# Optimization experiments

Measured on AMD Instinct MI355X. Metric: run time of the kernel, lower is better.

## Reference

```python
import jax, jax.numpy as jnp
import numpy as np

B, S, N = 8, 2048, 1024

def setup_inputs() -> dict:
    key = jax.random.key(0)
    k1, k2, k3 = jax.random.split(key, 3)
    outer = jax.random.normal(k1, (B, S, N), dtype=jnp.float32)
    extended_attention_mask = jnp.zeros((B, 1, S), dtype=jnp.float32)
    # torch Linear init scale ~ 1/sqrt(n)
    sc = 1.0 / np.sqrt(N)
    Wk = jax.random.normal(k2, (N, N), dtype=jnp.float32) * sc
    bk = jnp.zeros((N,), dtype=jnp.float32)
    Wq = jax.random.normal(k3, (N, N), dtype=jnp.float32) * sc
    bq = jnp.zeros((N,), dtype=jnp.float32)
    return {"outer": outer, "extended_attention_mask": extended_attention_mask,
            "Wk": Wk, "bk": bk, "Wq": Wq, "bq": bq}

def reference(outer, extended_attention_mask, Wk, bk, Wq, bq):
    # k = sigmoid(outer @ Wk^T + bk), q = sigmoid(outer @ Wq^T + bq)
    k = jax.nn.sigmoid(jnp.einsum('bsn,mn->bsm', outer, Wk) + bk)  # [B,S,N]
    q = jax.nn.sigmoid(jnp.einsum('bsn,mn->bsm', outer, Wq) + bq)  # [B,S,N]
    # scores: q @ k^T + mask -> [B,S,S]
    s = jnp.einsum('bqn,bkn->bqk', q, k) + extended_attention_mask
    attn = jax.nn.softmax(s, axis=-1)
    out = jnp.einsum('bqk,bkn->bqn', attn, outer)  # [B,S,N]
    return out.sum(-1)  # [B,S]
```

## Files before the change

### kernel.cpp

```cpp
#include <hip/hip_runtime.h>
#include <hip/hip_bf16.h>

#define BB 8
#define SS 2048
#define NN 1024
#define MT (BB*SS)
#define NPC 32

typedef __attribute__((ext_vector_type(8))) short bf16x8;
typedef __attribute__((ext_vector_type(4))) float f32x4;
typedef unsigned short u16;
typedef unsigned int u32;

__device__ __forceinline__ u16 f2bf(float f) {
  u32 u = __float_as_uint(f);
  u += 0x7fff + ((u >> 16) & 1);
  return (u16)(u >> 16);
}
__device__ __forceinline__ float bf2f(u16 h) {
  return __uint_as_float(((u32)h) << 16);
}

typedef __attribute__((address_space(1))) void GV;
typedef __attribute__((address_space(3))) void LV;
__device__ __forceinline__ void cp16(const void* g, void* l) {
  __builtin_amdgcn_global_load_lds((GV*)g, (LV*)l, 16, 0, 0);
}

__global__ __launch_bounds__(256) void prep_kernel(const float* __restrict__ outer,
                                                   const float* __restrict__ mask,
                                                   const float* __restrict__ Wq,
                                                   const float* __restrict__ Wk,
                                                   const float* __restrict__ bq,
                                                   const float* __restrict__ bk,
                                                   u16* __restrict__ Xb,
                                                   float* __restrict__ r,
                                                   float* __restrict__ kb,
                                                   u16* __restrict__ Wb,
                                                   float* __restrict__ bb) {
  int blk = blockIdx.x;
  if (blk < MT / 4) {
    int w = threadIdx.x >> 6, lane = threadIdx.x & 63;
    int row = blk * 4 + w;
    const float4* src = (const float4*)(outer + (size_t)row * NN);
    ushort4* dst = (ushort4*)(Xb + (size_t)row * NN);
    float s = 0.f;
#pragma unroll
    for (int u = 0; u < 4; u++) {
      int idx = lane + u * 64;
      float4 v = src[idx];
      ushort4 o;
      o.x = f2bf(v.x); o.y = f2bf(v.y); o.z = f2bf(v.z); o.w = f2bf(v.w);
      dst[idx] = o;
      s += (v.x + v.y) + (v.z + v.w);
    }
#pragma unroll
    for (int off = 1; off < 64; off <<= 1) s += __shfl_xor(s, off);
    if (lane == 0) { r[row] = s; kb[row] = mask[row]; }
  } else {
    int idx = (blk - MT / 4) * 256 + threadIdx.x;
    int e = idx * 4;
    int rowm = e >> 10;
    int col = e & 1023;
    const float* srcp = (rowm < NN) ? (Wq + (size_t)rowm * NN + col)
                                    : (Wk + (size_t)(rowm - NN) * NN + col);
    float4 v = *(const float4*)srcp;
    ushort4 o; o.x = f2bf(v.x); o.y = f2bf(v.y); o.z = f2bf(v.z); o.w = f2bf(v.w);
    *(ushort4*)(Wb + (size_t)e) = o;
    if (idx < 2 * NN) bb[idx] = (idx < NN) ? bq[idx] : bk[idx - NN];
  }
}

__global__ __launch_bounds__(256, 4) void gemm1_kernel(const u16* __restrict__ X,
                                                       const u16* __restrict__ W,
                                                       const float* __restrict__ bb,
                                                       u16* __restrict__ C,
                                                       float* __restrict__ kb) {
  __shared__ u16 lA[128 * 32];
  __shared__ u16 lB[128 * 32];
  int bid = blockIdx.x;
  int tn = ((bid & 7) << 1) | ((bid >> 3) & 1);
  int tm = bid >> 4;
  int tid = threadIdx.x;
  int w = tid >> 6, lane = tid & 63;
  int wr = w >> 1, wc = w & 1;
  int srow = tid >> 2;
  int gchunk = (tid & 3) ^ ((tid >> 3) & 3);
  const u16* gA = X + (size_t)(tm * 128 + srow) * NN + gchunk * 8;
  const u16* gB = W + (size_t)(tn * 128 + srow) * NN + gchunk * 8;
  u16* dA = &lA[srow * 32 + (tid & 3) * 8];
  u16* dB = &lB[srow * 32 + (tid & 3) * 8];
  int quad = lane >> 4;
  int rl = lane & 15;
  int sw = quad ^ ((rl >> 1) & 3);
  const u16* pa0 = &lA[(wr * 64 + rl) * 32 + sw * 8];
  const u16* pb0 = &lB[(wc * 64 + rl) * 32 + sw * 8];
  f32x4 acc[4][4] = {};
  for (int kk = 0; kk < NN; kk += 32) {
    cp16(gA, dA);
    cp16(gA + 64 * NN, dA + 64 * 32);
    cp16(gB, dB);
    cp16(gB + 64 * NN, dB + 64 * 32);
    gA += 32; gB += 32;
    __syncthreads();
    bf16x8 af[4], bf[4];
#pragma unroll
    for (int i = 0; i < 4; i++) af[i] = *(const bf16x8*)(pa0 + i * 16 * 32);
#pragma unroll
    for (int j = 0; j < 4; j++) bf[j] = *(const bf16x8*)(pb0 + j * 16 * 32);
#pragma unroll
    for (int i = 0; i < 4; i++)
#pragma unroll
      for (int j = 0; j < 4; j++)
        acc[i][j] = __builtin_amdgcn_mfma_f32_16x16x32_bf16(af[i], bf[j], acc[i][j], 0, 0, 0);
    __syncthreads();
  }
  int quad4 = quad * 4;
  int colb = tn * 128 + wc * 64 + rl;
  bool khalf = (tn >= 8);
#pragma unroll
  for (int i = 0; i < 4; i++) {
    float rsum[4] = {0.f, 0.f, 0.f, 0.f};
#pragma unroll
    for (int j = 0; j < 4; j++) {
      int col = colb + j * 16;
      float bias = bb[col];
#pragma unroll
      for (int rg = 0; rg < 4; rg++) {
        int row = tm * 128 + wr * 64 + i * 16 + quad4 + rg;
        float v = acc[i][j][rg] + bias;
        float sg = 1.0f / (1.0f + __expf(-v));
        u16 h = f2bf(sg - 0.5f);
        C[(size_t)row * 2048 + col] = h;
        rsum[rg] += bf2f(h);
      }
    }
    if (khalf) {
#pragma unroll
      for (int rg = 0; rg < 4; rg++) {
        float s = rsum[rg];
#pragma unroll
        for (int off = 1; off < 16; off <<= 1) s += __shfl_xor(s, off);
        if (rl == 0) {
          int row = tm * 128 + wr * 64 + i * 16 + quad4 + rg;
          atomicAdd(&kb[row], 0.5f * s);
        }
      }
    }
  }
}

__global__ __launch_bounds__(256, 4) void flash_kernel(const u16* __restrict__ C,
                                                       const float* __restrict__ kb,
                                                       const float* __restrict__ r,
                                                       float* __restrict__ pm,
                                                       float* __restrict__ pl,
                                                       float* __restrict__ pt) {
  __shared__ u16 lA[128 * 32];
  __shared__ u16 lB[128 * 32];
  int bid = blockIdx.x;
  int b  = bid & 7;
  int kc = (bid >> 3) & 15;
  int qt = bid >> 7;
  int tid = threadIdx.x;
  int w = tid >> 6, lane = tid & 63;
  int wr = w >> 1, wc = w & 1;
  int srow = tid >> 2;
  int gchunk = (tid & 3) ^ ((tid >> 3) & 3);
  int key0 = kc * 128;
  const u16* gA = C + (size_t)(b * SS + qt * 128 + srow) * 2048 + gchunk * 8;
  const u16* gB = C + (size_t)(b * SS + key0 + srow) * 2048 + 1024 + gchunk * 8;
  u16* dA = &lA[srow * 32 + (tid & 3) * 8];
  u16* dB = &lB[srow * 32 + (tid & 3) * 8];
  int quad = lane >> 4;
  int rl = lane & 15;
  int sw = quad ^ ((rl >> 1) & 3);
  const u16* pa0 = &lA[(wr * 64 + rl) * 32 + sw * 8];
  const u16* pb0 = &lB[(wc * 64 + rl) * 32 + sw * 8];

  f32x4 acc[4][4] = {};
  for (int kk = 0; kk < NN; kk += 32) {
    cp16(gA, dA);
    cp16(gA + 64 * 2048, dA + 64 * 32);
    cp16(gB, dB);
    cp16(gB + 64 * 2048, dB + 64 * 32);
    gA += 32; gB += 32;
    __syncthreads();
    bf16x8 af[4], bf[4];
#pragma unroll
    for (int i = 0; i < 4; i++) af[i] = *(const bf16x8*)(pa0 + i * 16 * 32);
#pragma unroll
    for (int j = 0; j < 4; j++) bf[j] = *(const bf16x8*)(pb0 + j * 16 * 32);
#pragma unroll
    for (int i = 0; i < 4; i++)
#pragma unroll
      for (int j = 0; j < 4; j++)
        acc[i][j] = __builtin_amdgcn_mfma_f32_16x16x32_bf16(af[i], bf[j], acc[i][j], 0, 0, 0);
    __syncthreads();
  }

  float kbv[4], rv[4];
  int colg = b * SS + key0 + wc * 64 + rl;
#pragma unroll
  for (int j = 0; j < 4; j++) { kbv[j] = kb[colg + j * 16]; rv[j] = r[colg + j * 16]; }
  int quad4 = quad * 4;
  int chunk = kc * 2 + wc;
#pragma unroll
  for (int i = 0; i < 4; i++) {
#pragma unroll
    for (int rg = 0; rg < 4; rg++) {
      float lg[4];
      float tmax = -1e30f;
#pragma unroll
      for (int j = 0; j < 4; j++) { lg[j] = acc[i][j][rg] + kbv[j]; tmax = fmaxf(tmax, lg[j]); }
#pragma unroll
      for (int off = 1; off < 16; off <<= 1) tmax = fmaxf(tmax, __shfl_xor(tmax, off));
      float rs = 0.f, rt = 0.f;
#pragma unroll
      for (int j = 0; j < 4; j++) {
        float p = __expf(lg[j] - tmax);
        rs += p; rt += p * rv[j];
      }
#pragma unroll
      for (int off = 1; off < 16; off <<= 1) { rs += __shfl_xor(rs, off); rt += __shfl_xor(rt, off); }
      if (rl == 0) {
        int grow = b * SS + qt * 128 + wr * 64 + i * 16 + quad4 + rg;
        pm[grow * NPC + chunk] = tmax;
        pl[grow * NPC + chunk] = rs;
        pt[grow * NPC + chunk] = rt;
      }
    }
  }
}

__global__ __launch_bounds__(256) void fixup_kernel(const float* __restrict__ pm,
                                                    const float* __restrict__ pl,
                                                    const float* __restrict__ pt,
                                                    float* __restrict__ out) {
  int row = blockIdx.x * 256 + threadIdx.x;
  float Mx = -1e30f;
#pragma unroll
  for (int c = 0; c < NPC; c++) Mx = fmaxf(Mx, pm[row * NPC + c]);
  float L = 0.f, T = 0.f;
#pragma unroll
  for (int c = 0; c < NPC; c++) {
    float a = __expf(pm[row * NPC + c] - Mx);
    L += pl[row * NPC + c] * a;
    T += pt[row * NPC + c] * a;
  }
  out[row] = T / L;
}

extern "C" void kernel_launch(void* const* d_in, const int* in_sizes, int n_in,
                              void* d_out, int out_size, void* d_ws, size_t ws_size,
                              hipStream_t stream) {
  const float* outer = (const float*)d_in[0];
  const float* mask  = (const float*)d_in[1];
  const float* Wk    = (const float*)d_in[2];
  const float* bk    = (const float*)d_in[3];
  const float* Wq    = (const float*)d_in[4];
  const float* bq    = (const float*)d_in[5];
  float* out = (float*)d_out;

  char* ws = (char*)d_ws;
  size_t off = 0;
  auto alloc = [&](size_t bytes) -> void* {
    void* p = ws + off;
    off = (off + bytes + 255) & ~(size_t)255;
    return p;
  };
  u16* Xb  = (u16*)alloc((size_t)MT * NN * 2);
  u16* Wb  = (u16*)alloc((size_t)2048 * NN * 2);
  u16* Cq  = (u16*)alloc((size_t)MT * 2048 * 2);
  float* bb = (float*)alloc(2048 * 4);
  float* rr = (float*)alloc((size_t)MT * 4);
  float* kb = (float*)alloc((size_t)MT * 4);
  float* pm = (float*)alloc((size_t)MT * NPC * 4);
  float* pl = (float*)alloc((size_t)MT * NPC * 4);
  float* pt = (float*)alloc((size_t)MT * NPC * 4);

  prep_kernel<<<dim3(MT / 4 + 2048), dim3(256), 0, stream>>>(outer, mask, Wq, Wk, bq, bk,
                                                             Xb, rr, kb, Wb, bb);
  gemm1_kernel<<<dim3(2048), dim3(256), 0, stream>>>(Xb, Wb, bb, Cq, kb);
  flash_kernel<<<dim3(2048), dim3(256), 0, stream>>>(Cq, kb, rr, pm, pl, pt);
  fixup_kernel<<<dim3(MT / 256), dim3(256), 0, stream>>>(pm, pl, pt, out);
}
```

Before: 295.5 us.

## Fuse fixup into flash kernel via last-block counter and remap gemm tiles

Removes the separate fixup kernel: each flash block bumps an atomic counter per (batch, query-tile), and the last of the 16 arriving blocks merges the partial max/sum/weighted-sum for its 128 rows. This saves one kernel launch and its reload of the partials, at the cost of a memset and fences. The gemm1 block-to-tile mapping is also changed so that blocks sharing an XCD get distinct M tiles and iterate over all N tiles, aiming at better L2 reuse of X. The launch-bounds occupancy hint drops from 4 to 3 blocks for gemm1 and flash, giving the compiler more registers.

```diff
diff --git a/kernel.cpp b/kernel.cpp
--- a/kernel.cpp
+++ b/kernel.cpp
@@ -46,8 +46,8 @@
     ushort4* dst = (ushort4*)(Xb + (size_t)row * NN);
     float s = 0.f;
 #pragma unroll
-    for (int u = 0; u < 4; u++) {
-      int idx = lane + u * 64;
+    for (int u2 = 0; u2 < 4; u2++) {
+      int idx = lane + u2 * 64;
       float4 v = src[idx];
       ushort4 o;
       o.x = f2bf(v.x); o.y = f2bf(v.y); o.z = f2bf(v.z); o.w = f2bf(v.w);
@@ -71,7 +71,7 @@
   }
 }
 
-__global__ __launch_bounds__(256, 4) void gemm1_kernel(const u16* __restrict__ X,
+__global__ __launch_bounds__(256, 3) void gemm1_kernel(const u16* __restrict__ X,
                                                        const u16* __restrict__ W,
                                                        const float* __restrict__ bb,
                                                        u16* __restrict__ C,
@@ -79,8 +79,10 @@
   __shared__ u16 lA[128 * 32];
   __shared__ u16 lB[128 * 32];
   int bid = blockIdx.x;
-  int tn = ((bid & 7) << 1) | ((bid >> 3) & 1);
-  int tm = bid >> 4;
+  int xcd = bid & 7;
+  int j = bid >> 3;
+  int tn = j & 15;
+  int tm = ((j >> 4) << 3) | xcd;
   int tid = threadIdx.x;
   int w = tid >> 6, lane = tid & 63;
   int wr = w >> 1, wc = w & 1;
@@ -107,12 +109,12 @@
 #pragma unroll
     for (int i = 0; i < 4; i++) af[i] = *(const bf16x8*)(pa0 + i * 16 * 32);
 #pragma unroll
-    for (int j = 0; j < 4; j++) bf[j] = *(const bf16x8*)(pb0 + j * 16 * 32);
+    for (int j2 = 0; j2 < 4; j2++) bf[j2] = *(const bf16x8*)(pb0 + j2 * 16 * 32);
 #pragma unroll
     for (int i = 0; i < 4; i++)
 #pragma unroll
-      for (int j = 0; j < 4; j++)
-        acc[i][j] = __builtin_amdgcn_mfma_f32_16x16x32_bf16(af[i], bf[j], acc[i][j], 0, 0, 0);
+      for (int j2 = 0; j2 < 4; j2++)
+        acc[i][j2] = __builtin_amdgcn_mfma_f32_16x16x32_bf16(af[i], bf[j2], acc[i][j2], 0, 0, 0);
     __syncthreads();
   }
   int quad4 = quad * 4;
@@ -122,13 +124,13 @@
   for (int i = 0; i < 4; i++) {
     float rsum[4] = {0.f, 0.f, 0.f, 0.f};
 #pragma unroll
-    for (int j = 0; j < 4; j++) {
-      int col = colb + j * 16;
+    for (int j2 = 0; j2 < 4; j2++) {
+      int col = colb + j2 * 16;
       float bias = bb[col];
 #pragma unroll
       for (int rg = 0; rg < 4; rg++) {
         int row = tm * 128 + wr * 64 + i * 16 + quad4 + rg;
-        float v = acc[i][j][rg] + bias;
+        float v = acc[i][j2][rg] + bias;
         float sg = 1.0f / (1.0f + __expf(-v));
         u16 h = f2bf(sg - 0.5f);
         C[(size_t)row * 2048 + col] = h;
@@ -150,14 +152,17 @@
   }
 }
 
-__global__ __launch_bounds__(256, 4) void flash_kernel(const u16* __restrict__ C,
+__global__ __launch_bounds__(256, 3) void flash_kernel(const u16* __restrict__ C,
                                                        const float* __restrict__ kb,
                                                        const float* __restrict__ r,
                                                        float* __restrict__ pm,
                                                        float* __restrict__ pl,
-                                                       float* __restrict__ pt) {
+                                                       float* __restrict__ pt,
+                                                       float* __restrict__ out,
+                                                       u32* __restrict__ fd) {
   __shared__ u16 lA[128 * 32];
   __shared__ u16 lB[128 * 32];
+  __shared__ int s_last;
   int bid = blockIdx.x;
   int b  = bid & 7;
   int kc = (bid >> 3) & 15;
@@ -231,24 +236,31 @@
       }
     }
   }
-}
-
-__global__ __launch_bounds__(256) void fixup_kernel(const float* __restrict__ pm,
-                                                    const float* __restrict__ pl,
-                                                    const float* __restrict__ pt,
-                                                    float* __restrict__ out) {
-  int row = blockIdx.x * 256 + threadIdx.x;
-  float Mx = -1e30f;
-#pragma unroll
-  for (int c = 0; c < NPC; c++) Mx = fmaxf(Mx, pm[row * NPC + c]);
-  float L = 0.f, T = 0.f;
-#pragma unroll
-  for (int c = 0; c < NPC; c++) {
-    float a = __expf(pm[row * NPC + c] - Mx);
-    L += pl[row * NPC + c] * a;
-    T += pt[row * NPC + c] * a;
-  }
-  out[row] = T / L;
+
+  __syncthreads();
+  if (tid == 0) {
+    __threadfence();
+    u32 old = atomicAdd(&fd[b * 16 + qt], 1u);
+    s_last = (old == 15u);
+  }
+  __syncthreads();
+  if (s_last) {
+    __threadfence();
+    if (tid < 128) {
+      int row = b * SS + qt * 128 + tid;
+      float Mx = -1e30f;
+#pragma unroll
+      for (int c = 0; c < NPC; c++) Mx = fmaxf(Mx, pm[row * NPC + c]);
+      float L = 0.f, T = 0.f;
+#pragma unroll
+      for (int c = 0; c < NPC; c++) {
+        float a = __expf(pm[row * NPC + c] - Mx);
+        L += pl[row * NPC + c] * a;
+        T += pt[row * NPC + c] * a;
+      }
+      out[row] = T / L;
+    }
+  }
 }
 
 extern "C" void kernel_launch(void* const* d_in, const int* in_sizes, int n_in,
@@ -278,10 +290,11 @@
   float* pm = (float*)alloc((size_t)MT * NPC * 4);
   float* pl = (float*)alloc((size_t)MT * NPC * 4);
   float* pt = (float*)alloc((size_t)MT * NPC * 4);
-
+  u32* fd  = (u32*)alloc(128 * 4);
+
+  hipMemsetAsync(fd, 0, 128 * 4, stream);
   prep_kernel<<<dim3(MT / 4 + 2048), dim3(256), 0, stream>>>(outer, mask, Wq, Wk, bq, bk,
                                                              Xb, rr, kb, Wb, bb);
   gemm1_kernel<<<dim3(2048), dim3(256), 0, stream>>>(Xb, Wb, bb, Cq, kb);
-  flash_kernel<<<dim3(2048), dim3(256), 0, stream>>>(Cq, kb, rr, pm, pl, pt);
-  fixup_kernel<<<dim3(MT / 256), dim3(256), 0, stream>>>(pm, pl, pt, out);
-}
+  flash_kernel<<<dim3(2048), dim3(256), 0, stream>>>(Cq, kb, rr, pm, pl, pt, out, fd);
+}
```

Measured after the change: 403.9 us. 1.37x slower.
